# Kernel tuning notes

Hardware: AMD Instinct MI355X
Metric: run time of the kernel (lower is better)

Reference implementation:

```python
import jax, jax.numpy as jnp
import numpy as np

NUM_EMBEDDINGS = 1024
EMBEDDING_DIM = 64
BETA = 0.25


def setup_inputs() -> dict:
    key = jax.random.key(0)
    k1, k2 = jax.random.split(key)
    z = jax.random.normal(k1, (64, 32, 32, EMBEDDING_DIM), dtype=jnp.float32)
    emb = jax.random.uniform(
        k2, (NUM_EMBEDDINGS, EMBEDDING_DIM), dtype=jnp.float32,
        minval=-1.0 / NUM_EMBEDDINGS, maxval=1.0 / NUM_EMBEDDINGS)
    return {"z": z, "emb": emb}


def reference(z, emb):
    zf = z.reshape(-1, EMBEDDING_DIM)                      # [N, D]
    # squared L2 distances via ||z||^2 - 2 z.e + ||e||^2  -> [N, K]
    distances = (jnp.sum(zf * zf, axis=1, keepdims=True)
                 - 2.0 * jnp.matmul(zf, emb.T)
                 + jnp.sum(emb * emb, axis=1))
    encoding_indices = jnp.argmin(distances, axis=1)       # [N]
    quantized = emb[encoding_indices].reshape(z.shape)     # [B, H, W, D]
    commitment_loss = BETA * jnp.mean((jax.lax.stop_gradient(quantized) - z) ** 2)
    codebook_loss = jnp.mean((quantized - jax.lax.stop_gradient(z)) ** 2)
    loss = commitment_loss + codebook_loss
    # straight-through estimator
    quantized = z + jax.lax.stop_gradient(quantized - z)
    return (quantized, loss)
```

## Files before the change

kernel.cpp:

```cpp
#include <hip/hip_runtime.h>
#include <stdint.h>

#define N_ROWS 65536
#define K_CODES 1024
#define D 64
#define OUT_ELEMS 4194304
#define LOSS_SCALE (1.25f / 4194304.0f)
#define ROWS_PER_BLOCK 256
#define GRID_DIST (N_ROWS / ROWS_PER_BLOCK)
#define SETS (ROWS_PER_BLOCK / 16)

typedef short short8 __attribute__((ext_vector_type(8)));
typedef float f32x4 __attribute__((ext_vector_type(4)));

__device__ __forceinline__ unsigned short f2bf(float f) {
    unsigned int u = __float_as_uint(f);
    return (unsigned short)((u + 0x7fffu + ((u >> 16) & 1u)) >> 16);
}
__device__ __forceinline__ short8 pack8(float4 a, float4 b) {
    short8 r;
    r[0] = f2bf(a.x); r[1] = f2bf(a.y); r[2] = f2bf(a.z); r[3] = f2bf(a.w);
    r[4] = f2bf(b.x); r[5] = f2bf(b.y); r[6] = f2bf(b.z); r[7] = f2bf(b.w);
    return r;
}

__global__ __launch_bounds__(512, 2) void vq_kernel(
        const float* __restrict__ z, const float* __restrict__ emb,
        float* __restrict__ out, float* __restrict__ partials) {
    const int tid = threadIdx.x;
    const int w = tid >> 6, lane = tid & 63;
    const int n = lane & 15, q = lane >> 4;
    __shared__ unsigned int sh_key[2][8][16];
    __shared__ float ps[8];

    const int r0 = blockIdx.x * ROWS_PER_BLOCK;

    float4 c0, c1, c2, c3;
    {
        const float* zr = z + (size_t)(r0 + n) * D + q * 8;
        c0 = *(const float4*)(zr);      c1 = *(const float4*)(zr + 4);
        c2 = *(const float4*)(zr + 32); c3 = *(const float4*)(zr + 36);
    }

    const int cbase = w * 128 + n;
    short8 cb0[8], cb1[8];
    float e2w[8];
#pragma unroll
    for (int ct = 0; ct < 8; ct++) {
        const float* er = emb + (size_t)(cbase + ct * 16) * D + q * 8;
        float4 g0 = *(const float4*)(er);      float4 g1 = *(const float4*)(er + 4);
        float4 g2 = *(const float4*)(er + 32); float4 g3 = *(const float4*)(er + 36);
        float e2p = g0.x*g0.x + g0.y*g0.y + g0.z*g0.z + g0.w*g0.w
                  + g1.x*g1.x + g1.y*g1.y + g1.z*g1.z + g1.w*g1.w
                  + g2.x*g2.x + g2.y*g2.y + g2.z*g2.z + g2.w*g2.w
                  + g3.x*g3.x + g3.y*g3.y + g3.z*g3.z + g3.w*g3.w;
        e2p += __shfl_xor(e2p, 16, 64);
        e2p += __shfl_xor(e2p, 32, 64);
        e2w[ct] = e2p + 1.0f;
        float4 m0 = {-2.f*g0.x, -2.f*g0.y, -2.f*g0.z, -2.f*g0.w};
        float4 m1 = {-2.f*g1.x, -2.f*g1.y, -2.f*g1.z, -2.f*g1.w};
        float4 m2 = {-2.f*g2.x, -2.f*g2.y, -2.f*g2.z, -2.f*g2.w};
        float4 m3 = {-2.f*g3.x, -2.f*g3.y, -2.f*g3.z, -2.f*g3.w};
        cb0[ct] = pack8(m0, m1);
        cb1[ct] = pack8(m2, m3);
    }

    float lossacc = 0.f;
    const float4* emb4 = (const float4*)emb;
    float4* o4 = (float4*)out;

    for (int s = 0; s < SETS; s++) {
        float z2p = c0.x*c0.x + c0.y*c0.y + c0.z*c0.z + c0.w*c0.w
                  + c1.x*c1.x + c1.y*c1.y + c1.z*c1.z + c1.w*c1.w
                  + c2.x*c2.x + c2.y*c2.y + c2.z*c2.z + c2.w*c2.w
                  + c3.x*c3.x + c3.y*c3.y + c3.z*c3.z + c3.w*c3.w;
        z2p += __shfl_xor(z2p, 16, 64);
        z2p += __shfl_xor(z2p, 32, 64);
        float z2r[4];
#pragma unroll
        for (int r = 0; r < 4; r++) z2r[r] = __shfl(z2p, q * 4 + r, 64);

        short8 alo = pack8(c0, c1), ahi = pack8(c2, c3);

        unsigned int best[4] = {~0u, ~0u, ~0u, ~0u};
#pragma unroll
        for (int ct = 0; ct < 8; ct++) {
            f32x4 acc = {e2w[ct], e2w[ct], e2w[ct], e2w[ct]};
            acc = __builtin_amdgcn_mfma_f32_16x16x32_bf16(alo, cb0[ct], acc, 0, 0, 0);
            acc = __builtin_amdgcn_mfma_f32_16x16x32_bf16(ahi, cb1[ct], acc, 0, 0, 0);
            const unsigned int id = (unsigned int)(cbase + ct * 16);
#pragma unroll
            for (int r = 0; r < 4; r++) {
                unsigned int key = (__float_as_uint(acc[r] + z2r[r]) & 0xFFFFFC00u) | id;
                best[r] = best[r] < key ? best[r] : key;
            }
        }
#pragma unroll
        for (int r = 0; r < 4; r++) {
#pragma unroll
            for (int x = 1; x < 16; x <<= 1) {
                unsigned int o = (unsigned int)__shfl_xor((int)best[r], x, 64);
                best[r] = o < best[r] ? o : best[r];
            }
        }
        if (n == 0)
            *(uint4*)&sh_key[s & 1][w][q << 2] =
                make_uint4(best[0], best[1], best[2], best[3]);

        float4 n0, n1, n2, n3;
        if (s < SETS - 1) {
            const float* zr = z + (size_t)(r0 + (s + 1) * 16 + n) * D + q * 8;
            n0 = *(const float4*)(zr);      n1 = *(const float4*)(zr + 4);
            n2 = *(const float4*)(zr + 32); n3 = *(const float4*)(zr + 36);
        }
        __syncthreads();

        if (tid < 256) {
            const int row = tid >> 4, unit = tid & 15;
            unsigned int km = sh_key[s & 1][0][row];
#pragma unroll
            for (int ww = 1; ww < 8; ww++) {
                unsigned int o = sh_key[s & 1][ww][row];
                km = o < km ? o : km;
            }
            int idx = (int)(km & 1023u);
            o4[(size_t)(r0 + s * 16 + row) * 16 + unit] = emb4[idx * 16 + unit];
            if (unit == 0)
                lossacc += __uint_as_float(km & 0xFFFFFC00u) - 1.0f;
        }
        c0 = n0; c1 = n1; c2 = n2; c3 = n3;
    }

#pragma unroll
    for (int off = 32; off > 0; off >>= 1)
        lossacc += __shfl_down(lossacc, off, 64);
    if (lane == 0) ps[w] = lossacc;
    __syncthreads();
    if (tid == 0) {
        float s8 = 0.f;
#pragma unroll
        for (int ww = 0; ww < 8; ww++) s8 += ps[ww];
        partials[blockIdx.x] = s8;
    }
}

__global__ __launch_bounds__(256) void loss_kernel(const float* __restrict__ partials,
                                                   float* __restrict__ loss) {
    float s = partials[threadIdx.x];
#pragma unroll
    for (int off = 32; off > 0; off >>= 1)
        s += __shfl_down(s, off, 64);
    __shared__ float ps[4];
    int wave = threadIdx.x >> 6, lane = threadIdx.x & 63;
    if (lane == 0) ps[wave] = s;
    __syncthreads();
    if (threadIdx.x == 0) loss[0] = (ps[0] + ps[1] + ps[2] + ps[3]) * LOSS_SCALE;
}

extern "C" void kernel_launch(void* const* d_in, const int* in_sizes, int n_in,
                              void* d_out, int out_size, void* d_ws, size_t ws_size,
                              hipStream_t stream) {
    const float* z = (const float*)d_in[0];
    const float* emb = (const float*)d_in[1];
    float* out = (float*)d_out;
    float* loss = out + OUT_ELEMS;
    float* partials = (float*)d_ws;

    vq_kernel<<<GRID_DIST, 512, 0, stream>>>(z, emb, out, partials);
    loss_kernel<<<1, 256, 0, stream>>>(partials, loss);
}
```

Before: 100.2 us.

## Drop per-row z norm from argmin, batch epilogue, halve rows per block

Removes the per-row ||z||^2 computation and shuffles from the argmin, since that term is constant within a row, and compares keys as floats with fminf instead of as biased unsigned keys. The per-set barrier and gather are replaced by one barrier after all sets, followed by a batched gather that also computes the exact squared-error loss from z and the selected codeword. Rows per block drop from 256 to 128, doubling the grid, with a launch-bounds occupancy hint of 4, and the loss kernel now sums 512 partials. In exchange, z is read twice, loads are no longer prefetched across sets, and float min over keys whose mantissa bits are masked could mis-order negative distances.

```diff
diff --git a/kernel.cpp b/kernel.cpp
--- a/kernel.cpp
+++ b/kernel.cpp
@@ -6,7 +6,7 @@
 #define D 64
 #define OUT_ELEMS 4194304
 #define LOSS_SCALE (1.25f / 4194304.0f)
-#define ROWS_PER_BLOCK 256
+#define ROWS_PER_BLOCK 128
 #define GRID_DIST (N_ROWS / ROWS_PER_BLOCK)
 #define SETS (ROWS_PER_BLOCK / 16)
 
@@ -24,23 +24,15 @@
     return r;
 }
 
-__global__ __launch_bounds__(512, 2) void vq_kernel(
+__global__ __launch_bounds__(512, 4) void vq_kernel(
         const float* __restrict__ z, const float* __restrict__ emb,
         float* __restrict__ out, float* __restrict__ partials) {
     const int tid = threadIdx.x;
     const int w = tid >> 6, lane = tid & 63;
     const int n = lane & 15, q = lane >> 4;
-    __shared__ unsigned int sh_key[2][8][16];
+    __shared__ float sh_key[SETS][8][16];
     __shared__ float ps[8];
-
     const int r0 = blockIdx.x * ROWS_PER_BLOCK;
-
-    float4 c0, c1, c2, c3;
-    {
-        const float* zr = z + (size_t)(r0 + n) * D + q * 8;
-        c0 = *(const float4*)(zr);      c1 = *(const float4*)(zr + 4);
-        c2 = *(const float4*)(zr + 32); c3 = *(const float4*)(zr + 36);
-    }
 
     const int cbase = w * 128 + n;
     short8 cb0[8], cb1[8];
@@ -56,7 +48,7 @@
                   + g3.x*g3.x + g3.y*g3.y + g3.z*g3.z + g3.w*g3.w;
         e2p += __shfl_xor(e2p, 16, 64);
         e2p += __shfl_xor(e2p, 32, 64);
-        e2w[ct] = e2p + 1.0f;
+        e2w[ct] = e2p;
         float4 m0 = {-2.f*g0.x, -2.f*g0.y, -2.f*g0.z, -2.f*g0.w};
         float4 m1 = {-2.f*g1.x, -2.f*g1.y, -2.f*g1.z, -2.f*g1.w};
         float4 m2 = {-2.f*g2.x, -2.f*g2.y, -2.f*g2.z, -2.f*g2.w};
@@ -65,24 +57,14 @@
         cb1[ct] = pack8(m2, m3);
     }
 
-    float lossacc = 0.f;
-    const float4* emb4 = (const float4*)emb;
-    float4* o4 = (float4*)out;
-
     for (int s = 0; s < SETS; s++) {
-        float z2p = c0.x*c0.x + c0.y*c0.y + c0.z*c0.z + c0.w*c0.w
-                  + c1.x*c1.x + c1.y*c1.y + c1.z*c1.z + c1.w*c1.w
-                  + c2.x*c2.x + c2.y*c2.y + c2.z*c2.z + c2.w*c2.w
-                  + c3.x*c3.x + c3.y*c3.y + c3.z*c3.z + c3.w*c3.w;
-        z2p += __shfl_xor(z2p, 16, 64);
-        z2p += __shfl_xor(z2p, 32, 64);
-        float z2r[4];
-#pragma unroll
-        for (int r = 0; r < 4; r++) z2r[r] = __shfl(z2p, q * 4 + r, 64);
-
+        const float* zr = z + (size_t)(r0 + s * 16 + n) * D + q * 8;
+        float4 c0 = *(const float4*)(zr);      float4 c1 = *(const float4*)(zr + 4);
+        float4 c2 = *(const float4*)(zr + 32); float4 c3 = *(const float4*)(zr + 36);
         short8 alo = pack8(c0, c1), ahi = pack8(c2, c3);
 
-        unsigned int best[4] = {~0u, ~0u, ~0u, ~0u};
+        float best[4] = {__builtin_huge_valf(), __builtin_huge_valf(),
+                         __builtin_huge_valf(), __builtin_huge_valf()};
 #pragma unroll
         for (int ct = 0; ct < 8; ct++) {
             f32x4 acc = {e2w[ct], e2w[ct], e2w[ct], e2w[ct]};
@@ -91,46 +73,41 @@
             const unsigned int id = (unsigned int)(cbase + ct * 16);
 #pragma unroll
             for (int r = 0; r < 4; r++) {
-                unsigned int key = (__float_as_uint(acc[r] + z2r[r]) & 0xFFFFFC00u) | id;
-                best[r] = best[r] < key ? best[r] : key;
+                float kf = __uint_as_float((__float_as_uint(acc[r]) & 0xFFFFFC00u) | id);
+                best[r] = __builtin_fminf(best[r], kf);
             }
         }
 #pragma unroll
-        for (int r = 0; r < 4; r++) {
+        for (int r = 0; r < 4; r++)
 #pragma unroll
-            for (int x = 1; x < 16; x <<= 1) {
-                unsigned int o = (unsigned int)__shfl_xor((int)best[r], x, 64);
-                best[r] = o < best[r] ? o : best[r];
-            }
-        }
+            for (int x = 1; x < 16; x <<= 1)
+                best[r] = __builtin_fminf(best[r], __shfl_xor(best[r], x, 64));
         if (n == 0)
-            *(uint4*)&sh_key[s & 1][w][q << 2] =
-                make_uint4(best[0], best[1], best[2], best[3]);
+            *(float4*)&sh_key[s][w][q << 2] =
+                make_float4(best[0], best[1], best[2], best[3]);
+    }
+    __syncthreads();
 
-        float4 n0, n1, n2, n3;
-        if (s < SETS - 1) {
-            const float* zr = z + (size_t)(r0 + (s + 1) * 16 + n) * D + q * 8;
-            n0 = *(const float4*)(zr);      n1 = *(const float4*)(zr + 4);
-            n2 = *(const float4*)(zr + 32); n3 = *(const float4*)(zr + 36);
-        }
-        __syncthreads();
-
-        if (tid < 256) {
-            const int row = tid >> 4, unit = tid & 15;
-            unsigned int km = sh_key[s & 1][0][row];
+    float lossacc = 0.f;
+    const float4* emb4 = (const float4*)emb;
+    const float4* z4 = (const float4*)z + (size_t)r0 * 16;
+    float4* o4 = (float4*)out + (size_t)r0 * 16;
 #pragma unroll
-            for (int ww = 1; ww < 8; ww++) {
-                unsigned int o = sh_key[s & 1][ww][row];
-                km = o < km ? o : km;
-            }
-            int idx = (int)(km & 1023u);
-            o4[(size_t)(r0 + s * 16 + row) * 16 + unit] = emb4[idx * 16 + unit];
-            if (unit == 0)
-                lossacc += __uint_as_float(km & 0xFFFFFC00u) - 1.0f;
-        }
-        c0 = n0; c1 = n1; c2 = n2; c3 = n3;
+    for (int it = 0; it < 4; it++) {
+        int u = it * 512 + tid;
+        int row = u >> 4, unit = u & 15;
+        int s = row >> 4, ri = row & 15;
+        float km = sh_key[s][0][ri];
+#pragma unroll
+        for (int ww = 1; ww < 8; ww++)
+            km = __builtin_fminf(km, sh_key[s][ww][ri]);
+        int idx = (int)(__float_as_uint(km) & 1023u);
+        float4 qv = emb4[idx * 16 + unit];
+        float4 zv = z4[u];
+        o4[u] = qv;
+        float dx = qv.x - zv.x, dy = qv.y - zv.y, dz = qv.z - zv.z, dw = qv.w - zv.w;
+        lossacc += dx * dx + dy * dy + dz * dz + dw * dw;
     }
-
 #pragma unroll
     for (int off = 32; off > 0; off >>= 1)
         lossacc += __shfl_down(lossacc, off, 64);
@@ -146,7 +123,7 @@
 
 __global__ __launch_bounds__(256) void loss_kernel(const float* __restrict__ partials,
                                                    float* __restrict__ loss) {
-    float s = partials[threadIdx.x];
+    float s = partials[threadIdx.x] + partials[threadIdx.x + 256];
 #pragma unroll
     for (int off = 32; off > 0; off >>= 1)
         s += __shfl_down(s, off, 64);
```

New measurement: 125.8 us. +25.6%, slower.
